# Optimization experiments

Measured on AMD Instinct MI355X. Metric: run time of the kernel, lower is better.

Reference implementation:

```python
import jax, jax.numpy as jnp
import numpy as np

N, F_IN, H, C, E, G, OUT = 50000, 128, 4, 64, 800000, 128, 8

def _glorot(key, shape):
    lim = float(np.sqrt(6.0 / (shape[0] + shape[-1] if len(shape) == 2 else shape[-1] + 1)))
    return jax.random.uniform(key, shape, jnp.float32, -lim, lim)

def setup_inputs() -> dict:
    key = jax.random.key(0)
    ks = jax.random.split(key, 12)
    x = jax.random.normal(ks[0], (N, F_IN), jnp.float32)
    edge_index = jax.random.randint(ks[1], (2, E), 0, N, jnp.int64)
    batch = jnp.sort(jax.random.randint(ks[2], (N,), 0, G, jnp.int64))
    return {
        "x": x, "edge_index": edge_index, "batch": batch,
        "W1": _glorot(ks[3], (F_IN, H * C)),
        "a1s": _glorot(ks[4], (H, C)), "a1d": _glorot(ks[5], (H, C)),
        "b1": jnp.zeros((H * C,), jnp.float32),
        "W2": _glorot(ks[6], (H * C, H * C)),
        "a2s": _glorot(ks[7], (H, C)), "a2d": _glorot(ks[8], (H, C)),
        "b2": jnp.zeros((C,), jnp.float32),
        "fc_w": _glorot(ks[9], (C, OUT)),
        "fc_b": jnp.zeros((OUT,), jnp.float32),
    }

def _gat_conv(x, src, dst, W, a_src, a_dst, bias, concat):
    # x: [N, in]; src/dst: [E'] (self-loops already appended, PyG default)
    n = x.shape[0]
    h = (x @ W).reshape(n, H, C)                       # [N, H, C]
    alpha_src = (h * a_src).sum(-1)                    # [N, H]
    alpha_dst = (h * a_dst).sum(-1)                    # [N, H]
    e = alpha_src[src] + alpha_dst[dst]                # [E', H]
    e = jax.nn.leaky_relu(e, 0.2)
    # neighbor softmax grouped by destination node
    m = jax.ops.segment_max(e, dst, num_segments=n)    # [N, H]
    ex = jnp.exp(e - m[dst])
    denom = jax.ops.segment_sum(ex, dst, num_segments=n)
    alpha = ex / (denom[dst] + 1e-16)                  # [E', H]
    msg = h[src] * alpha[:, :, None]                   # [E', H, C]
    out = jax.ops.segment_sum(msg, dst, num_segments=n)  # [N, H, C]
    out = out.reshape(n, H * C) if concat else out.mean(axis=1)
    return out + bias

def reference(x, edge_index, batch, W1, a1s, a1d, b1, W2, a2s, a2d, b2, fc_w, fc_b):
    n = x.shape[0]
    loop = jnp.arange(n, dtype=edge_index.dtype)
    src = jnp.concatenate([edge_index[0], loop])
    dst = jnp.concatenate([edge_index[1], loop])
    h = _gat_conv(x, src, dst, W1, a1s, a1d, b1, concat=True)
    h = jax.nn.elu(h)                                  # activation, dropout p=0
    h = _gat_conv(h, src, dst, W2, a2s, a2d, b2, concat=False)
    # global mean pool over graphs
    sums = jax.ops.segment_sum(h, batch, num_segments=G)
    cnts = jax.ops.segment_sum(jnp.ones((n,), h.dtype), batch, num_segments=G)
    pooled = sums / jnp.maximum(cnts, 1.0)[:, None]    # [G, C]
    return pooled @ fc_w + fc_b                        # [G, OUT]
```

## Files before the change

kernel.cpp:

```cpp
#include <hip/hip_runtime.h>
#include <hip/hip_bf16.h>
#include <cstddef>
#include <cstdint>

#define NN 50000
#define MPAD 50048
#define F_IN 128
#define NH 4
#define NC 64
#define NE 800000
#define NG 128
#define NOUT 8
#define HC 256
#define EP (NE + NN)
#define NREP 16

typedef unsigned short ushort_t;
typedef _Float16 f16;
typedef __attribute__((ext_vector_type(2))) _Float16 f16x2;
typedef __attribute__((ext_vector_type(8))) _Float16 f16x8;
typedef __attribute__((ext_vector_type(4))) float f32x4;

__device__ __forceinline__ float lrelu02(float x) { return x > 0.0f ? x : 0.2f * x; }
__device__ __forceinline__ float elu1(float x)    { return x > 0.0f ? x : expm1f(x); }

__device__ __forceinline__ ushort_t f2h_bits(float f) {
    f16 h = (f16)f;
    union { f16 h; ushort_t u; } cv; cv.h = h;
    return cv.u;
}
__device__ __forceinline__ uint32_t pack2h(float a, float b) {
    union { f16 h[2]; uint32_t u; } cv;
    cv.h[0] = (f16)a; cv.h[1] = (f16)b;
    return cv.u;
}
__device__ __forceinline__ f16x2 as_h2(uint32_t q) {
    union { uint32_t u; f16x2 h; } cv; cv.u = q;
    return cv.h;
}
__device__ __forceinline__ void h2_unpack(uint32_t q, float& lo, float& hi) {
    union { uint32_t u; f16 h[2]; } cv; cv.u = q;
    lo = (float)cv.h[0];
    hi = (float)cv.h[1];
}

__device__ __forceinline__ float fdot2f(f16x2 a, f16x2 b, float c) {
#if __has_builtin(__builtin_amdgcn_fdot2)
    return __builtin_amdgcn_fdot2(a, b, c, false);
#else
    float d;
    asm("v_dot2_f32_f16 %0, %1, %2, %3" : "=v"(d) : "v"(a), "v"(b), "v"(c));
    return d;
#endif
}
__device__ __forceinline__ uint32_t permb(uint32_t a, uint32_t b, uint32_t s) {
    return __builtin_amdgcn_perm(a, b, s);
}
#define SEL_E 0x01000504u
#define SEL_O 0x03020706u

__device__ __forceinline__ void gld16(const void* g, void* l) {
    __builtin_amdgcn_global_load_lds(
        (const __attribute__((address_space(1))) unsigned int*)g,
        (__attribute__((address_space(3))) unsigned int*)l, 16, 0, 0);
}

#define XN4 (NN * F_IN / 4)
#define NW (F_IN * HC + HC * HC)
__global__ void prep_kernel(const int* __restrict__ edst,
                            const float* __restrict__ x,
                            const float* __restrict__ W1,
                            const float* __restrict__ W2,
                            int* __restrict__ deg,
                            int* __restrict__ rank,
                            f16* __restrict__ xh,
                            f16* __restrict__ w1t, f16* __restrict__ w2t) {
    int idx = blockIdx.x * blockDim.x + threadIdx.x;
    if (idx < EP) {
        int d = (idx < NE) ? edst[idx] : (idx - NE);
        rank[idx] = atomicAdd(&deg[d], 1);
        return;
    }
    idx -= EP;
    if (idx < XN4) {
        float4 v = ((const float4*)x)[idx];
        f16 o[4] = {(f16)v.x, (f16)v.y, (f16)v.z, (f16)v.w};
        *(uint2*)(xh + idx * 4) = *(const uint2*)o;
        return;
    }
    idx -= XN4;
    const int n1 = F_IN * HC;
    if (idx < n1) {
        int k = idx / HC, n = idx % HC;
        w1t[n * F_IN + k] = (f16)W1[idx];
    } else if (idx < NW) {
        int i2 = idx - n1;
        int k = i2 / HC, n = i2 % HC;
        w2t[n * HC + k] = (f16)W2[i2];
    }
}

__global__ __launch_bounds__(256) void scan_p1(const int* __restrict__ deg,
                                               int* __restrict__ partials) {
    __shared__ int lds[256];
    int b = blockIdx.x, t = threadIdx.x;
    int i0 = b * 1024 + t * 4;
    int s = 0;
#pragma unroll
    for (int j = 0; j < 4; j++) { int i = i0 + j; if (i < NN) s += deg[i]; }
    lds[t] = s;
    __syncthreads();
    for (int o = 128; o; o >>= 1) { if (t < o) lds[t] += lds[t + o]; __syncthreads(); }
    if (t == 0) partials[b] = lds[0];
}

__global__ __launch_bounds__(256) void scan_p3(const int* __restrict__ deg,
                                               const int* __restrict__ partials,
                                               int* __restrict__ offs) {
    __shared__ int lds[256];
    __shared__ int base_s;
    int b = blockIdx.x, t = threadIdx.x;
    if (t == 0) {
        int s = 0;
        for (int i = 0; i < b; i++) s += partials[i];
        base_s = s;
        if (b == 0) offs[0] = 0;
    }
    int i0 = b * 1024 + t * 4;
    int v[4]; int s = 0;
#pragma unroll
    for (int j = 0; j < 4; j++) { int i = i0 + j; v[j] = (i < NN) ? deg[i] : 0; s += v[j]; }
    lds[t] = s;
    __syncthreads();
    for (int o = 1; o < 256; o <<= 1) {
        int x = (t >= o) ? lds[t - o] : 0;
        __syncthreads();
        lds[t] += x;
        __syncthreads();
    }
    int run = base_s + (lds[t] - s);
#pragma unroll
    for (int j = 0; j < 4; j++) { run += v[j]; int i = i0 + j; if (i < NN) offs[i + 1] = run; }
}

__global__ void edge_fill(const int* __restrict__ esrc, const int* __restrict__ edst,
                          const int* __restrict__ offs, const int* __restrict__ rank,
                          int* __restrict__ csr) {
    int e = blockIdx.x * blockDim.x + threadIdx.x;
    if (e >= EP) return;
    int s, d;
    if (e < NE) { s = esrc[e]; d = edst[e]; } else { s = d = e - NE; }
    csr[offs[d] + rank[e]] = s;
}

__global__ __launch_bounds__(256, 3) void gemm_gat(
        const f16* __restrict__ A, const f16* __restrict__ BT,
        const float* __restrict__ a_s, const float* __restrict__ a_d,
        ushort_t* __restrict__ hf2, float* __restrict__ asrc,
        float* __restrict__ adst, int M, int K) {
    __shared__ alignas(16) char smem[33792];
    f16* lA = (f16*)smem;
    f16* lB = (f16*)smem + 4096;

    int t = threadIdx.x;
    int wave = t >> 6, lane = t & 63;
    int wm = wave >> 1, wn = wave & 1;
    int quad = lane >> 4, l15 = lane & 15;
    int tileM = blockIdx.x * 128;
    int by = blockIdx.y;

    f32x4 acc[4][4];
#pragma unroll
    for (int f = 0; f < 4; f++)
#pragma unroll
        for (int g = 0; g < 4; g++) acc[f][g] = (f32x4){0.f, 0.f, 0.f, 0.f};

    for (int k0 = 0; k0 < K; k0 += 32) {
        __syncthreads();
#pragma unroll
        for (int i = 0; i < 2; i++) {
            int c = wave * 2 + i;
            int row = c * 16 + (lane >> 2);
            int kk = k0 + (lane & 3) * 8;
            gld16(A + (size_t)(tileM + row) * K + kk, &lA[c * 512]);
            gld16(BT + (size_t)(by * 128 + row) * K + kk, &lB[c * 512]);
        }
        __syncthreads();

        f16x8 ah[4], bh[4];
#pragma unroll
        for (int f = 0; f < 4; f++)
            ah[f] = *(const f16x8*)&lA[(wm * 64 + f * 16 + l15) * 32 + quad * 8];
#pragma unroll
        for (int g = 0; g < 4; g++)
            bh[g] = *(const f16x8*)&lB[(wn * 64 + g * 16 + l15) * 32 + quad * 8];
#pragma unroll
        for (int f = 0; f < 4; f++)
#pragma unroll
            for (int g = 0; g < 4; g++)
                acc[f][g] = __builtin_amdgcn_mfma_f32_16x16x32_f16(ah[f], bh[g], acc[f][g], 0, 0, 0);
    }

    int head = (by << 1) | wn;
    float as_v[4], ad_v[4];
#pragma unroll
    for (int g = 0; g < 4; g++) {
        as_v[g] = a_s[head * 64 + g * 16 + l15];
        ad_v[g] = a_d[head * 64 + g * 16 + l15];
    }
#pragma unroll
    for (int f = 0; f < 4; f++) {
#pragma unroll
        for (int r = 0; r < 4; r++) {
            float ps = acc[f][0][r] * as_v[0] + acc[f][1][r] * as_v[1]
                     + acc[f][2][r] * as_v[2] + acc[f][3][r] * as_v[3];
            float pd = acc[f][0][r] * ad_v[0] + acc[f][1][r] * ad_v[1]
                     + acc[f][2][r] * ad_v[2] + acc[f][3][r] * ad_v[3];
#pragma unroll
            for (int o = 1; o < 16; o <<= 1) {
                ps += __shfl_xor(ps, o);
                pd += __shfl_xor(pd, o);
            }
            int row = tileM + wm * 64 + f * 16 + quad * 4 + r;
            if (l15 == 0 && row < M) {
                asrc[row * 4 + head] = ps;
                adst[row * 4 + head] = pd;
            }
        }
    }

    __syncthreads();
    ushort_t* lC2u = (ushort_t*)smem;
    const uint32_t* lC2d = (const uint32_t*)smem;
#pragma unroll
    for (int f = 0; f < 4; f++)
#pragma unroll
        for (int g = 0; g < 4; g++)
#pragma unroll
            for (int r = 0; r < 4; r++)
                lC2u[(wm * 64 + f * 16 + quad * 4 + r) * 132 + (g * 16 + l15) * 2 + wn] =
                    f2h_bits(acc[f][g][r]);
    __syncthreads();
    uint32_t* hb2 = (uint32_t*)hf2;
#pragma unroll
    for (int it = 0; it < 32; it++) {
        int row = wave * 32 + it;
        uint32_t v = lC2d[row * 66 + lane];
        hb2[(size_t)(tileM + row) * 128 + by * 64 + lane] = v;
    }
}

template <int CONCAT>
__device__ void gat_node_fullwave(const ushort_t* __restrict__ hf2,
                                  const float* __restrict__ asrc,
                                  const float* __restrict__ adst,
                                  const int* __restrict__ offs,
                                  const int* __restrict__ csr,
                                  const int* __restrict__ gb,
                                  const float* __restrict__ bias,
                                  f16* __restrict__ oh,
                                  float* __restrict__ of,
                                  int node, int lane, uint2* lwF) {
    int start = offs[node];
    int deg = offs[node + 1] - start;
    float4 ad = *(const float4*)(adst + node * 4);

    float w0, w1, w2, w3;
    float m0, m1, m2, m3, i0, i1, i2, i3;
    int msrc = 0;

    if (deg <= 64) {
        float t0 = -1e30f, t1 = -1e30f, t2 = -1e30f, t3 = -1e30f;
        if (lane < deg) {
            int sidx = csr[start + lane];
            float4 as = *(const float4*)(asrc + sidx * 4);
            t0 = lrelu02(as.x + ad.x);
            t1 = lrelu02(as.y + ad.y);
            t2 = lrelu02(as.z + ad.z);
            t3 = lrelu02(as.w + ad.w);
            msrc = sidx;
        }
        m0 = t0; m1 = t1; m2 = t2; m3 = t3;
#pragma unroll
        for (int o = 1; o < 64; o <<= 1) {
            m0 = fmaxf(m0, __shfl_xor(m0, o));
            m1 = fmaxf(m1, __shfl_xor(m1, o));
            m2 = fmaxf(m2, __shfl_xor(m2, o));
            m3 = fmaxf(m3, __shfl_xor(m3, o));
        }
        w0 = __expf(t0 - m0);
        w1 = __expf(t1 - m1);
        w2 = __expf(t2 - m2);
        w3 = __expf(t3 - m3);
        float s0 = w0, s1 = w1, s2 = w2, s3 = w3;
#pragma unroll
        for (int o = 1; o < 64; o <<= 1) {
            s0 += __shfl_xor(s0, o);
            s1 += __shfl_xor(s1, o);
            s2 += __shfl_xor(s2, o);
            s3 += __shfl_xor(s3, o);
        }
        i0 = 1.0f / (s0 + 1e-16f);
        i1 = 1.0f / (s1 + 1e-16f);
        i2 = 1.0f / (s2 + 1e-16f);
        i3 = 1.0f / (s3 + 1e-16f);
        w0 *= i0; w1 *= i1; w2 *= i2; w3 *= i3;
    } else {
        m0 = m1 = m2 = m3 = -1e30f;
        float s0 = 0.f, s1 = 0.f, s2 = 0.f, s3 = 0.f;
        float e0 = 0.f, e1 = 0.f, e2 = 0.f, e3 = 0.f;
        for (int j = lane; j < deg; j += 64) {
            int sidx = csr[start + j];
            float4 as = *(const float4*)(asrc + sidx * 4);
            float t0 = lrelu02(as.x + ad.x);
            float t1 = lrelu02(as.y + ad.y);
            float t2 = lrelu02(as.z + ad.z);
            float t3 = lrelu02(as.w + ad.w);
            if (j == lane) { e0 = t0; e1 = t1; e2 = t2; e3 = t3; msrc = sidx; }
            float nm;
            nm = fmaxf(m0, t0); s0 = s0 * __expf(m0 - nm) + __expf(t0 - nm); m0 = nm;
            nm = fmaxf(m1, t1); s1 = s1 * __expf(m1 - nm) + __expf(t1 - nm); m1 = nm;
            nm = fmaxf(m2, t2); s2 = s2 * __expf(m2 - nm) + __expf(t2 - nm); m2 = nm;
            nm = fmaxf(m3, t3); s3 = s3 * __expf(m3 - nm) + __expf(t3 - nm); m3 = nm;
        }
        for (int o = 32; o; o >>= 1) {
            float om, os, nm;
            om = __shfl_xor(m0, o); os = __shfl_xor(s0, o);
            nm = fmaxf(m0, om); s0 = s0 * __expf(m0 - nm) + os * __expf(om - nm); m0 = nm;
            om = __shfl_xor(m1, o); os = __shfl_xor(s1, o);
            nm = fmaxf(m1, om); s1 = s1 * __expf(m1 - nm) + os * __expf(om - nm); m1 = nm;
            om = __shfl_xor(m2, o); os = __shfl_xor(s2, o);
            nm = fmaxf(m2, om); s2 = s2 * __expf(m2 - nm) + os * __expf(om - nm); m2 = nm;
            om = __shfl_xor(m3, o); os = __shfl_xor(s3, o);
            nm = fmaxf(m3, om); s3 = s3 * __expf(m3 - nm) + os * __expf(om - nm); m3 = nm;
        }
        i0 = 1.0f / (s0 + 1e-16f);
        i1 = 1.0f / (s1 + 1e-16f);
        i2 = 1.0f / (s2 + 1e-16f);
        i3 = 1.0f / (s3 + 1e-16f);
        w0 = __expf(e0 - m0) * i0;
        w1 = __expf(e1 - m1) * i1;
        w2 = __expf(e2 - m2) * i2;
        w3 = __expf(e3 - m3) * i3;
    }

    lwF[lane] = (uint2){pack2h(w0, w1), pack2h(w2, w3)};

    int hp = lane >> 5;
    const uint32_t* lwu = (const uint32_t*)lwF;
    float aE0 = 0.f, aO0 = 0.f, aE1 = 0.f, aO1 = 0.f;
    float c0a = 0.f, c0b = 0.f, c1a = 0.f, c1b = 0.f;
    const uint32_t* hb = (const uint32_t*)hf2 + lane * 2;
    int jmax = deg < 64 ? deg : 64;

    int j = 0;
    if (CONCAT) {
        for (; j + 4 <= jmax; j += 4) {
            int s0 = __builtin_amdgcn_readlane(msrc, j);
            int s1 = __builtin_amdgcn_readlane(msrc, j + 1);
            int s2 = __builtin_amdgcn_readlane(msrc, j + 2);
            int s3 = __builtin_amdgcn_readlane(msrc, j + 3);
            uint2 q0 = *(const uint2*)(hb + (size_t)s0 * 128);
            uint2 q1 = *(const uint2*)(hb + (size_t)s1 * 128);
            uint2 q2 = *(const uint2*)(hb + (size_t)s2 * 128);
            uint2 q3 = *(const uint2*)(hb + (size_t)s3 * 128);
            uint32_t wA = lwu[(j + 0) * 2 + hp];
            uint32_t wB = lwu[(j + 1) * 2 + hp];
            uint32_t wC = lwu[(j + 2) * 2 + hp];
            uint32_t wD = lwu[(j + 3) * 2 + hp];
            uint32_t weAB = permb(wA, wB, SEL_E), woAB = permb(wA, wB, SEL_O);
            uint32_t weCD = permb(wC, wD, SEL_E), woCD = permb(wC, wD, SEL_O);
            uint32_t xeAB = permb(q0.x, q1.x, SEL_E), xoAB = permb(q0.x, q1.x, SEL_O);
            uint32_t yeAB = permb(q0.y, q1.y, SEL_E), yoAB = permb(q0.y, q1.y, SEL_O);
            uint32_t xeCD = permb(q2.x, q3.x, SEL_E), xoCD = permb(q2.x, q3.x, SEL_O);
            uint32_t yeCD = permb(q2.y, q3.y, SEL_E), yoCD = permb(q2.y, q3.y, SEL_O);
            aE0 = fdot2f(as_h2(xeAB), as_h2(weAB), aE0);
            aO0 = fdot2f(as_h2(xoAB), as_h2(woAB), aO0);
            aE1 = fdot2f(as_h2(yeAB), as_h2(weAB), aE1);
            aO1 = fdot2f(as_h2(yoAB), as_h2(woAB), aO1);
            aE0 = fdot2f(as_h2(xeCD), as_h2(weCD), aE0);
            aO0 = fdot2f(as_h2(xoCD), as_h2(woCD), aO0);
            aE1 = fdot2f(as_h2(yeCD), as_h2(weCD), aE1);
            aO1 = fdot2f(as_h2(yeCD), as_h2(woCD), aO1);
        }
        for (; j < jmax; j++) {
            int sidx = __builtin_amdgcn_readlane(msrc, j);
            f16x2 wh = as_h2(lwu[j * 2 + hp]);
            uint2 q = *(const uint2*)(hb + (size_t)sidx * 128);
            f16x2 qx = as_h2(q.x), qy = as_h2(q.y);
            aE0 += (float)qx[0] * (float)wh[0];
            aO0 += (float)qx[1] * (float)wh[1];
            aE1 += (float)qy[0] * (float)wh[0];
            aO1 += (float)qy[1] * (float)wh[1];
        }
    } else {
        for (; j + 4 <= jmax; j += 4) {
            int s0 = __builtin_amdgcn_readlane(msrc, j);
            int s1 = __builtin_amdgcn_readlane(msrc, j + 1);
            int s2 = __builtin_amdgcn_readlane(msrc, j + 2);
            int s3 = __builtin_amdgcn_readlane(msrc, j + 3);
            uint2 q0 = *(const uint2*)(hb + (size_t)s0 * 128);
            uint2 q1 = *(const uint2*)(hb + (size_t)s1 * 128);
            uint2 q2 = *(const uint2*)(hb + (size_t)s2 * 128);
            uint2 q3 = *(const uint2*)(hb + (size_t)s3 * 128);
            f16x2 w0v = as_h2(lwu[(j + 0) * 2 + hp]);
            f16x2 w1v = as_h2(lwu[(j + 1) * 2 + hp]);
            f16x2 w2v = as_h2(lwu[(j + 2) * 2 + hp]);
            f16x2 w3v = as_h2(lwu[(j + 3) * 2 + hp]);
            c0a = fdot2f(as_h2(q0.x), w0v, c0a);
            c1a = fdot2f(as_h2(q0.y), w0v, c1a);
            c0b = fdot2f(as_h2(q1.x), w1v, c0b);
            c1b = fdot2f(as_h2(q1.y), w1v, c1b);
            c0a = fdot2f(as_h2(q2.x), w2v, c0a);
            c1a = fdot2f(as_h2(q2.y), w2v, c1a);
            c0b = fdot2f(as_h2(q3.x), w3v, c0b);
            c1b = fdot2f(as_h2(q3.y), w3v, c1b);
        }
        for (; j < jmax; j++) {
            int sidx = __builtin_amdgcn_readlane(msrc, j);
            f16x2 wh = as_h2(lwu[j * 2 + hp]);
            uint2 q = *(const uint2*)(hb + (size_t)sidx * 128);
            c0a = fdot2f(as_h2(q.x), wh, c0a);
            c1a = fdot2f(as_h2(q.y), wh, c1a);
        }
    }
    for (int jj = 64; jj < deg; jj++) {
        int sidx = csr[start + jj];
        float4 as = *(const float4*)(asrc + sidx * 4);
        float u0 = __expf(lrelu02(as.x + ad.x) - m0) * i0;
        float u1 = __expf(lrelu02(as.y + ad.y) - m1) * i1;
        float u2 = __expf(lrelu02(as.z + ad.z) - m2) * i2;
        float u3 = __expf(lrelu02(as.w + ad.w) - m3) * i3;
        float ue = hp ? u2 : u0;
        float uo = hp ? u3 : u1;
        uint2 q = *(const uint2*)(hb + (size_t)sidx * 128);
        float xl, xh2, yl, yh;
        h2_unpack(q.x, xl, xh2);
        h2_unpack(q.y, yl, yh);
        if (CONCAT) {
            aE0 += ue * xl;
            aO0 += uo * xh2;
            aE1 += ue * yl;
            aO1 += uo * yh;
        } else {
            c0a += ue * xl + uo * xh2;
            c1a += ue * yl + uo * yh;
        }
    }

    int c0 = (lane & 31) * 2;
    int he = hp * 2, ho = hp * 2 + 1;
    if (CONCAT) {
        size_t base = (size_t)node * HC;
        float vE0 = elu1(aE0 + bias[he * 64 + c0]);
        float vE1 = elu1(aE1 + bias[he * 64 + c0 + 1]);
        float vO0 = elu1(aO0 + bias[ho * 64 + c0]);
        float vO1 = elu1(aO1 + bias[ho * 64 + c0 + 1]);
        f16 pe[2] = {(f16)vE0, (f16)vE1};
        f16 po[2] = {(f16)vO0, (f16)vO1};
        *(uint32_t*)(oh + base + he * 64 + c0) = *(const uint32_t*)pe;
        *(uint32_t*)(oh + base + ho * 64 + c0) = *(const uint32_t*)po;
    } else {
        float s0 = c0a + c0b;
        float s1 = c1a + c1b;
        s0 += __shfl_xor(s0, 32);
        s1 += __shfl_xor(s1, 32);
        if (hp == 0) {
            int g = gb[node];
            atomicAdd(of + g * 64 + c0, 0.25f * s0);
            atomicAdd(of + g * 64 + c0 + 1, 0.25f * s1);
        }
    }
}

template <int CONCAT>
__global__ __launch_bounds__(256, 4) void gat_agg(const ushort_t* __restrict__ hf2,
                                                  const float* __restrict__ asrc,
                                                  const float* __restrict__ adst,
                                                  const int* __restrict__ offs,
                                                  const int* __restrict__ csr,
                                                  const int* __restrict__ gb,
                                                  const float* __restrict__ bias,
                                                  f16* __restrict__ oh,
                                                  float* __restrict__ of) {
    __shared__ uint4 lw4[4][64];
    __shared__ float part[2][64];
    __shared__ int oks[4];
    int wave = threadIdx.x >> 6, lane = threadIdx.x & 63;
    int grp = lane >> 5, l31 = lane & 31;
    int hp = (lane >> 4) & 1;
    int nbase = blockIdx.x * 8 + wave * 2;
    int node = nbase + grp;
    int start = offs[node];
    int deg = offs[node + 1] - start;

    float* ofr = of + (size_t)(blockIdx.x & (NREP - 1)) * NG * 64;

    bool ok = __all(deg <= 32);
    bool useLds = false;
    int g_first = 0, g_last = 0;
    if (!CONCAT) {
        if (threadIdx.x < 128) ((float*)part)[threadIdx.x] = 0.f;
        if (lane == 0) oks[wave] = ok ? 1 : 0;
        __syncthreads();
        useLds = oks[0] && oks[1] && oks[2] && oks[3];
        g_first = gb[blockIdx.x * 8];
        g_last  = gb[blockIdx.x * 8 + 7];
    }

    if (!ok) {
        uint2* lwF = (uint2*)&lw4[wave][0];
        gat_node_fullwave<CONCAT>(hf2, asrc, adst, offs, csr, gb, bias, oh, ofr,
                                  nbase, lane, lwF);
        gat_node_fullwave<CONCAT>(hf2, asrc, adst, offs, csr, gb, bias, oh, ofr,
                                  nbase + 1, lane, lwF);
        return;
    }

    const uint4* hq = (const uint4*)hf2;
    int msrc = 0;
    bool act = l31 < deg;
    if (act) msrc = csr[start + l31];

    int b0 = grp * 32;
    int i0 = __shfl(msrc, b0 + 0);
    int i1 = __shfl(msrc, b0 + 1);
    int i2 = __shfl(msrc, b0 + 2);
    int i3 = __shfl(msrc, b0 + 3);
    int i4 = __shfl(msrc, b0 + 4);
    int i5 = __shfl(msrc, b0 + 5);
    int i6 = __shfl(msrc, b0 + 6);
    int i7 = __shfl(msrc, b0 + 7);
    uint4 q0 = hq[(uint32_t)i0 * 32u + l31];
    uint4 q1 = hq[(uint32_t)i1 * 32u + l31];
    uint4 q2 = hq[(uint32_t)i2 * 32u + l31];
    uint4 q3 = hq[(uint32_t)i3 * 32u + l31];
    uint4 r0 = hq[(uint32_t)i4 * 32u + l31];
    uint4 r1 = hq[(uint32_t)i5 * 32u + l31];
    uint4 r2 = hq[(uint32_t)i6 * 32u + l31];
    uint4 r3 = hq[(uint32_t)i7 * 32u + l31];

    float4 ad = *(const float4*)(adst + (size_t)node * 4);
    float t0 = -1e30f, t1 = -1e30f, t2 = -1e30f, t3 = -1e30f;
    if (act) {
        float4 as = *(const float4*)(asrc + (size_t)msrc * 4);
        t0 = lrelu02(as.x + ad.x);
        t1 = lrelu02(as.y + ad.y);
        t2 = lrelu02(as.z + ad.z);
        t3 = lrelu02(as.w + ad.w);
    }
    float m0 = t0, m1 = t1, m2 = t2, m3 = t3;
#pragma unroll
    for (int o = 1; o < 32; o <<= 1) {
        m0 = fmaxf(m0, __shfl_xor(m0, o));
        m1 = fmaxf(m1, __shfl_xor(m1, o));
        m2 = fmaxf(m2, __shfl_xor(m2, o));
        m3 = fmaxf(m3, __shfl_xor(m3, o));
    }
    float w0 = __expf(t0 - m0);
    float w1 = __expf(t1 - m1);
    float w2 = __expf(t2 - m2);
    float w3 = __expf(t3 - m3);
    float s0 = w0, s1 = w1, s2 = w2, s3 = w3;
#pragma unroll
    for (int o = 1; o < 32; o <<= 1) {
        s0 += __shfl_xor(s0, o);
        s1 += __shfl_xor(s1, o);
        s2 += __shfl_xor(s2, o);
        s3 += __shfl_xor(s3, o);
    }
    w0 *= 1.0f / (s0 + 1e-16f);
    w1 *= 1.0f / (s1 + 1e-16f);
    w2 *= 1.0f / (s2 + 1e-16f);
    w3 *= 1.0f / (s3 + 1e-16f);

    lw4[wave][lane] = (uint4){(uint32_t)msrc, pack2h(w0, w1),
                              (uint32_t)msrc, pack2h(w2, w3)};

    const uint2* lwp = (const uint2*)&lw4[wave][grp * 32];
    int c0 = (l31 & 15) * 4;
    int deg4 = (deg + 3) & ~3;

    uint32_t wy0 = lwp[0 * 2 + hp].y;
    uint32_t wy1 = lwp[1 * 2 + hp].y;
    uint32_t wy2 = lwp[2 * 2 + hp].y;
    uint32_t wy3 = lwp[3 * 2 + hp].y;
    uint32_t wz0 = lwp[4 * 2 + hp].y;
    uint32_t wz1 = lwp[5 * 2 + hp].y;
    uint32_t wz2 = lwp[6 * 2 + hp].y;
    uint32_t wz3 = lwp[7 * 2 + hp].y;

    if (CONCAT) {
        float aE0 = 0.f, aE1 = 0.f, aE2 = 0.f, aE3 = 0.f;
        float aO0 = 0.f, aO1 = 0.f, aO2 = 0.f, aO3 = 0.f;
#define CPAIR(A0, A1, W0, W1)                                                  \
        {                                                                      \
            uint32_t we = permb(W0, W1, SEL_E);                                \
            uint32_t wo = permb(W0, W1, SEL_O);                                \
            aE0 = fdot2f(as_h2(permb(A0.x, A1.x, SEL_E)), as_h2(we), aE0);     \
            aO0 = fdot2f(as_h2(permb(A0.x, A1.x, SEL_O)), as_h2(wo), aO0);     \
            aE1 = fdot2f(as_h2(permb(A0.y, A1.y, SEL_E)), as_h2(we), aE1);     \
            aO1 = fdot2f(as_h2(permb(A0.y, A1.y, SEL_O)), as_h2(wo), aO1);     \
            aE2 = fdot2f(as_h2(permb(A0.z, A1.z, SEL_E)), as_h2(we), aE2);     \
            aO2 = fdot2f(as_h2(permb(A0.z, A1.z, SEL_O)), as_h2(wo), aO2);     \
            aE3 = fdot2f(as_h2(permb(A0.w, A1.w, SEL_E)), as_h2(we), aE3);     \
            aO3 = fdot2f(as_h2(permb(A0.w, A1.w, SEL_O)), as_h2(wo), aO3);     \
        }
        int j = 0;
        for (;;) {
            CPAIR(q0, q1, wy0, wy1)
            CPAIR(q2, q3, wy2, wy3)
            {
                int p = j + 8;
                if (p < deg4) {
                    uint2 n0 = lwp[(p + 0) * 2 + hp];
                    uint2 n1 = lwp[(p + 1) * 2 + hp];
                    uint2 n2 = lwp[(p + 2) * 2 + hp];
                    uint2 n3 = lwp[(p + 3) * 2 + hp];
                    wy0 = n0.y; wy1 = n1.y; wy2 = n2.y; wy3 = n3.y;
                    q0 = hq[n0.x * 32u + l31];
                    q1 = hq[n1.x * 32u + l31];
                    q2 = hq[n2.x * 32u + l31];
                    q3 = hq[n3.x * 32u + l31];
                }
            }
            j += 4;
            if (j >= deg4) break;
            CPAIR(r0, r1, wz0, wz1)
            CPAIR(r2, r3, wz2, wz3)
            {
                int p = j + 8;
                if (p < deg4) {
                    uint2 n0 = lwp[(p + 0) * 2 + hp];
                    uint2 n1 = lwp[(p + 1) * 2 + hp];
                    uint2 n2 = lwp[(p + 2) * 2 + hp];
                    uint2 n3 = lwp[(p + 3) * 2 + hp];
                    wz0 = n0.y; wz1 = n1.y; wz2 = n2.y; wz3 = n3.y;
                    r0 = hq[n0.x * 32u + l31];
                    r1 = hq[n1.x * 32u + l31];
                    r2 = hq[n2.x * 32u + l31];
                    r3 = hq[n3.x * 32u + l31];
                }
            }
            j += 4;
            if (j >= deg4) break;
        }
#undef CPAIR
        int he = hp * 2, ho = hp * 2 + 1;
        size_t base = (size_t)node * HC;
        float4 bE = *(const float4*)(bias + he * 64 + c0);
        float4 bO = *(const float4*)(bias + ho * 64 + c0);
        f16 pe[4] = {(f16)elu1(aE0 + bE.x), (f16)elu1(aE1 + bE.y),
                     (f16)elu1(aE2 + bE.z), (f16)elu1(aE3 + bE.w)};
        f16 po[4] = {(f16)elu1(aO0 + bO.x), (f16)elu1(aO1 + bO.y),
                     (f16)elu1(aO2 + bO.z), (f16)elu1(aO3 + bO.w)};
        *(uint2*)(oh + base + he * 64 + c0) = *(const uint2*)pe;
        *(uint2*)(oh + base + ho * 64 + c0) = *(const uint2*)po;
    } else {
        float a0 = 0.f, a1 = 0.f, a2 = 0.f, a3 = 0.f;
        float b0f = 0.f, b1f = 0.f, b2f = 0.f, b3f = 0.f;
        int j = 0;
        for (;;) {
            {
                f16x2 wvA = as_h2(wy0), wvB = as_h2(wy1);
                f16x2 wvC = as_h2(wy2), wvD = as_h2(wy3);
                a0 = fdot2f(as_h2(q0.x), wvA, a0);
                a1 = fdot2f(as_h2(q0.y), wvA, a1);
                a2 = fdot2f(as_h2(q0.z), wvA, a2);
                a3 = fdot2f(as_h2(q0.w), wvA, a3);
                b0f = fdot2f(as_h2(q1.x), wvB, b0f);
                b1f = fdot2f(as_h2(q1.y), wvB, b1f);
                b2f = fdot2f(as_h2(q1.z), wvB, b2f);
                b3f = fdot2f(as_h2(q1.w), wvB, b3f);
                a0 = fdot2f(as_h2(q2.x), wvC, a0);
                a1 = fdot2f(as_h2(q2.y), wvC, a1);
                a2 = fdot2f(as_h2(q2.z), wvC, a2);
                a3 = fdot2f(as_h2(q2.w), wvC, a3);
                b0f = fdot2f(as_h2(q3.x), wvD, b0f);
                b1f = fdot2f(as_h2(q3.y), wvD, b1f);
                b2f = fdot2f(as_h2(q3.z), wvD, b2f);
                b3f = fdot2f(as_h2(q3.w), wvD, b3f);
            }
            {
                int p = j + 8;
                if (p < deg4) {
                    uint2 n0 = lwp[(p + 0) * 2 + hp];
                    uint2 n1 = lwp[(p + 1) * 2 + hp];
                    uint2 n2 = lwp[(p + 2) * 2 + hp];
                    uint2 n3 = lwp[(p + 3) * 2 + hp];
                    wy0 = n0.y; wy1 = n1.y; wy2 = n2.y; wy3 = n3.y;
                    q0 = hq[n0.x * 32u + l31];
                    q1 = hq[n1.x * 32u + l31];
                    q2 = hq[n2.x * 32u + l31];
                    q3 = hq[n3.x * 32u + l31];
                }
            }
            j += 4;
            if (j >= deg4) break;
            {
                f16x2 wvA = as_h2(wz0), wvB = as_h2(wz1);
                f16x2 wvC = as_h2(wz2), wvD = as_h2(wz3);
                a0 = fdot2f(as_h2(r0.x), wvA, a0);
                a1 = fdot2f(as_h2(r0.y), wvA, a1);
                a2 = fdot2f(as_h2(r0.z), wvA, a2);
                a3 = fdot2f(as_h2(r0.w), wvA, a3);
                b0f = fdot2f(as_h2(r1.x), wvB, b0f);
                b1f = fdot2f(as_h2(r1.y), wvB, b1f);
                b2f = fdot2f(as_h2(r1.z), wvB, b2f);
                b3f = fdot2f(as_h2(r1.w), wvB, b3f);
                a0 = fdot2f(as_h2(r2.x), wvC, a0);
                a1 = fdot2f(as_h2(r2.y), wvC, a1);
                a2 = fdot2f(as_h2(r2.z), wvC, a2);
                a3 = fdot2f(as_h2(r2.w), wvC, a3);
                b0f = fdot2f(as_h2(r3.x), wvD, b0f);
                b1f = fdot2f(as_h2(r3.y), wvD, b1f);
                b2f = fdot2f(as_h2(r3.z), wvD, b2f);
                b3f = fdot2f(as_h2(r3.w), wvD, b3f);
            }
            {
                int p = j + 8;
                if (p < deg4) {
                    uint2 n0 = lwp[(p + 0) * 2 + hp];
                    uint2 n1 = lwp[(p + 1) * 2 + hp];
                    uint2 n2 = lwp[(p + 2) * 2 + hp];
                    uint2 n3 = lwp[(p + 3) * 2 + hp];
                    wz0 = n0.y; wz1 = n1.y; wz2 = n2.y; wz3 = n3.y;
                    r0 = hq[n0.x * 32u + l31];
                    r1 = hq[n1.x * 32u + l31];
                    r2 = hq[n2.x * 32u + l31];
                    r3 = hq[n3.x * 32u + l31];
                }
            }
            j += 4;
            if (j >= deg4) break;
        }
        float u0 = a0 + b0f, u1 = a1 + b1f, u2 = a2 + b2f, u3 = a3 + b3f;
        u0 += __shfl_xor(u0, 16);
        u1 += __shfl_xor(u1, 16);
        u2 += __shfl_xor(u2, 16);
        u3 += __shfl_xor(u3, 16);
        float o0 = 0.25f * u0, o1 = 0.25f * u1, o2 = 0.25f * u2, o3 = 0.25f * u3;
        int g = gb[node];
        if (hp == 0) {
            bool inLds = useLds && (g == g_first || g == g_last);
            if (inLds) {
                int slot = (g != g_first) ? 1 : 0;
                atomicAdd(&part[slot][c0 + 0], o0);
                atomicAdd(&part[slot][c0 + 1], o1);
                atomicAdd(&part[slot][c0 + 2], o2);
                atomicAdd(&part[slot][c0 + 3], o3);
            } else {
                float* pb = ofr + g * 64 + c0;
                atomicAdd(pb + 0, o0);
                atomicAdd(pb + 1, o1);
                atomicAdd(pb + 2, o2);
                atomicAdd(pb + 3, o3);
            }
        }
        if (useLds) {
            __syncthreads();
            int t = threadIdx.x;
            if (t < 64) {
                atomicAdd(ofr + g_first * 64 + t, part[0][t]);
            } else if (t < 128 && g_last != g_first) {
                atomicAdd(ofr + g_last * 64 + (t - 64), part[1][t - 64]);
            }
        }
    }
}

__global__ void fc_kernel(const float* __restrict__ pool,
                          const int* __restrict__ batch,
                          const float* __restrict__ b2,
                          const float* __restrict__ fc_w, const float* __restrict__ fc_b,
                          float* __restrict__ out) {
    int idx = blockIdx.x * blockDim.x + threadIdx.x;
    if (idx >= NG * NOUT) return;
    int g = idx >> 3, o = idx & 7;
    int lo = 0, hi = NN;
    while (lo < hi) { int mid = (lo + hi) >> 1; if (batch[mid] < g) lo = mid + 1; else hi = mid; }
    int lo2 = lo, hi2 = NN;
    while (lo2 < hi2) { int mid = (lo2 + hi2) >> 1; if (batch[mid] < g + 1) lo2 = mid + 1; else hi2 = mid; }
    float inv = 1.0f / fmaxf((float)(lo2 - lo), 1.0f);
    float s = 0.f;
#pragma unroll
    for (int c = 0; c < 64; c++) {
        float v = 0.f;
#pragma unroll
        for (int r = 0; r < NREP; r++) v += pool[((size_t)r * NG + g) * 64 + c];
        s += (v * inv + b2[c]) * fc_w[c * 8 + o];
    }
    out[idx] = s + fc_b[o];
}

extern "C" void kernel_launch(void* const* d_in, const int* in_sizes, int n_in,
                              void* d_out, int out_size, void* d_ws, size_t ws_size,
                              hipStream_t stream) {
    const float* x    = (const float*)d_in[0];
    const int*   ei   = (const int*)d_in[1];
    const int*   batch= (const int*)d_in[2];
    const float* W1   = (const float*)d_in[3];
    const float* a1s  = (const float*)d_in[4];
    const float* a1d  = (const float*)d_in[5];
    const float* b1   = (const float*)d_in[6];
    const float* W2   = (const float*)d_in[7];
    const float* a2s  = (const float*)d_in[8];
    const float* a2d  = (const float*)d_in[9];
    const float* b2   = (const float*)d_in[10];
    const float* fc_w = (const float*)d_in[11];
    const float* fc_b = (const float*)d_in[12];
    float* out = (float*)d_out;

    char* p = (char*)d_ws;
    auto alloc = [&](size_t bytes) -> char* {
        char* r = p; p += (bytes + 255) & ~(size_t)255; return r;
    };
    int*   deg     = (int*)alloc((size_t)NN * 4);
    float* pool    = (float*)alloc((size_t)NREP * NG * 64 * 4);
    size_t zero_bytes = (size_t)(p - (char*)d_ws);
    int*   offs    = (int*)alloc((size_t)(NN + 1) * 4);
    int*   partials= (int*)alloc(64 * 4);
    int*   csr     = (int*)alloc((size_t)EP * 4);
    int*   rank    = (int*)alloc((size_t)EP * 4);
    float* asrc    = (float*)alloc((size_t)NN * 4 * 4);
    float* adst    = (float*)alloc((size_t)NN * 4 * 4);
    ushort_t* hf2  = (ushort_t*)alloc((size_t)MPAD * HC * 2);
    f16*   xh      = (f16*)alloc((size_t)MPAD * F_IN * 2);
    f16*   act     = (f16*)alloc((size_t)MPAD * HC * 2);
    f16*   w1t     = (f16*)alloc((size_t)HC * F_IN * 2);
    f16*   w2t     = (f16*)alloc((size_t)HC * HC * 2);

    hipMemsetAsync(d_ws, 0, zero_bytes, stream);

    int prep_n = EP + XN4 + NW;
    prep_kernel<<<(prep_n + 255) / 256, 256, 0, stream>>>(
        ei + NE, x, W1, W2, deg, rank, xh, w1t, w2t);
    scan_p1<<<49, 256, 0, stream>>>(deg, partials);
    scan_p3<<<49, 256, 0, stream>>>(deg, partials, offs);
    edge_fill<<<(EP + 255) / 256, 256, 0, stream>>>(ei, ei + NE, offs, rank, csr);

    dim3 gg((NN + 127) / 128, HC / 128);
    int nb8 = (NN + 7) / 8;

    gemm_gat<<<gg, 256, 0, stream>>>(xh, w1t, a1s, a1d, hf2, asrc, adst, NN, F_IN);
    gat_agg<1><<<nb8, 256, 0, stream>>>(hf2, asrc, adst, offs, csr, batch, b1, act, nullptr);
    gemm_gat<<<gg, 256, 0, stream>>>(act, w2t, a2s, a2d, hf2, asrc, adst, NN, HC);
    gat_agg<0><<<nb8, 256, 0, stream>>>(hf2, asrc, adst, offs, csr, batch, b2, nullptr, pool);
    fc_kernel<<<(NG * NOUT + 255) / 256, 256, 0, stream>>>(pool, batch, b2, fc_w, fc_b, out);
}
```

Measured before the change: 346.1 us.

## Fuse CSR edge fill into first GEMM launch and widen GEMM K-tile with swizzle

Removes the separate edge_fill launch by appending extra blocks to the first gemm_gat grid that scatter edges into the CSR array, so the fill runs alongside the layer-1 GEMM. The GEMM K step doubles from 32 to 64 with an XOR-swizzled LDS layout to cut barriers per K and avoid LDS bank conflicts, and the grid becomes 1D. It also fixes a wrong operand (ye instead of yo) in the unrolled aggregation dot product, which changes the numerical result.

```diff
diff --git a/kernel.cpp b/kernel.cpp
--- a/kernel.cpp
+++ b/kernel.cpp
@@ -143,31 +143,36 @@
     for (int j = 0; j < 4; j++) { run += v[j]; int i = i0 + j; if (i < NN) offs[i + 1] = run; }
 }
 
-__global__ void edge_fill(const int* __restrict__ esrc, const int* __restrict__ edst,
-                          const int* __restrict__ offs, const int* __restrict__ rank,
-                          int* __restrict__ csr) {
-    int e = blockIdx.x * blockDim.x + threadIdx.x;
-    if (e >= EP) return;
-    int s, d;
-    if (e < NE) { s = esrc[e]; d = edst[e]; } else { s = d = e - NE; }
-    csr[offs[d] + rank[e]] = s;
-}
-
 __global__ __launch_bounds__(256, 3) void gemm_gat(
         const f16* __restrict__ A, const f16* __restrict__ BT,
         const float* __restrict__ a_s, const float* __restrict__ a_d,
         ushort_t* __restrict__ hf2, float* __restrict__ asrc,
-        float* __restrict__ adst, int M, int K) {
+        float* __restrict__ adst, int M, int K, int gemmBlocks,
+        const int* __restrict__ esrc, const int* __restrict__ edst,
+        const int* __restrict__ offs, const int* __restrict__ rank,
+        int* __restrict__ csr) {
     __shared__ alignas(16) char smem[33792];
+
+    int bid = blockIdx.x;
+    if (bid >= gemmBlocks) {
+        int e = (bid - gemmBlocks) * 256 + threadIdx.x;
+        if (e < EP) {
+            int s, d;
+            if (e < NE) { s = esrc[e]; d = edst[e]; } else { s = d = e - NE; }
+            csr[offs[d] + rank[e]] = s;
+        }
+        return;
+    }
+
     f16* lA = (f16*)smem;
-    f16* lB = (f16*)smem + 4096;
+    f16* lB = (f16*)smem + 8192;
 
     int t = threadIdx.x;
     int wave = t >> 6, lane = t & 63;
     int wm = wave >> 1, wn = wave & 1;
     int quad = lane >> 4, l15 = lane & 15;
-    int tileM = blockIdx.x * 128;
-    int by = blockIdx.y;
+    int tileM = (bid >> 1) * 128;
+    int by = bid & 1;
 
     f32x4 acc[4][4];
 #pragma unroll
@@ -175,30 +180,39 @@
 #pragma unroll
         for (int g = 0; g < 4; g++) acc[f][g] = (f32x4){0.f, 0.f, 0.f, 0.f};
 
-    for (int k0 = 0; k0 < K; k0 += 32) {
+    int swl = ((lane & 7) ^ (lane >> 3)) * 8;
+    int rsw = l15 & 7;
+
+    for (int k0 = 0; k0 < K; k0 += 64) {
         __syncthreads();
 #pragma unroll
-        for (int i = 0; i < 2; i++) {
-            int c = wave * 2 + i;
-            int row = c * 16 + (lane >> 2);
-            int kk = k0 + (lane & 3) * 8;
+        for (int i = 0; i < 4; i++) {
+            int c = wave * 4 + i;
+            int row = c * 8 + (lane >> 3);
+            int kk = k0 + swl;
             gld16(A + (size_t)(tileM + row) * K + kk, &lA[c * 512]);
             gld16(BT + (size_t)(by * 128 + row) * K + kk, &lB[c * 512]);
         }
         __syncthreads();
 
-        f16x8 ah[4], bh[4];
-#pragma unroll
-        for (int f = 0; f < 4; f++)
-            ah[f] = *(const f16x8*)&lA[(wm * 64 + f * 16 + l15) * 32 + quad * 8];
-#pragma unroll
-        for (int g = 0; g < 4; g++)
-            bh[g] = *(const f16x8*)&lB[(wn * 64 + g * 16 + l15) * 32 + quad * 8];
-#pragma unroll
-        for (int f = 0; f < 4; f++)
+#pragma unroll
+        for (int h = 0; h < 2; h++) {
+            f16x8 ah[4], bh[4];
+#pragma unroll
+            for (int f = 0; f < 4; f++)
+                ah[f] = *(const f16x8*)&lA[(wm * 64 + f * 16 + l15) * 64 +
+                                           (((h * 4 + quad) ^ rsw) * 8)];
 #pragma unroll
             for (int g = 0; g < 4; g++)
-                acc[f][g] = __builtin_amdgcn_mfma_f32_16x16x32_f16(ah[f], bh[g], acc[f][g], 0, 0, 0);
+                bh[g] = *(const f16x8*)&lB[(wn * 64 + g * 16 + l15) * 64 +
+                                           (((h * 4 + quad) ^ rsw) * 8)];
+#pragma unroll
+            for (int f = 0; f < 4; f++)
+#pragma unroll
+                for (int g = 0; g < 4; g++)
+                    acc[f][g] = __builtin_amdgcn_mfma_f32_16x16x32_f16(
+                        ah[f], bh[g], acc[f][g], 0, 0, 0);
+        }
     }
 
     int head = (by << 1) | wn;
@@ -381,7 +395,7 @@
             aE0 = fdot2f(as_h2(xeCD), as_h2(weCD), aE0);
             aO0 = fdot2f(as_h2(xoCD), as_h2(woCD), aO0);
             aE1 = fdot2f(as_h2(yeCD), as_h2(weCD), aE1);
-            aO1 = fdot2f(as_h2(yeCD), as_h2(woCD), aO1);
+            aO1 = fdot2f(as_h2(yoCD), as_h2(woCD), aO1);
         }
         for (; j < jmax; j++) {
             int sidx = __builtin_amdgcn_readlane(msrc, j);
@@ -837,14 +851,18 @@
         ei + NE, x, W1, W2, deg, rank, xh, w1t, w2t);
     scan_p1<<<49, 256, 0, stream>>>(deg, partials);
     scan_p3<<<49, 256, 0, stream>>>(deg, partials, offs);
-    edge_fill<<<(EP + 255) / 256, 256, 0, stream>>>(ei, ei + NE, offs, rank, csr);
-
-    dim3 gg((NN + 127) / 128, HC / 128);
+
+    int gemmB = ((NN + 127) / 128) * 2;
+    int fillB = (EP + 255) / 256;
     int nb8 = (NN + 7) / 8;
 
-    gemm_gat<<<gg, 256, 0, stream>>>(xh, w1t, a1s, a1d, hf2, asrc, adst, NN, F_IN);
+    gemm_gat<<<gemmB + fillB, 256, 0, stream>>>(
+        xh, w1t, a1s, a1d, hf2, asrc, adst, NN, F_IN, gemmB,
+        ei, ei + NE, offs, rank, csr);
     gat_agg<1><<<nb8, 256, 0, stream>>>(hf2, asrc, adst, offs, csr, batch, b1, act, nullptr);
-    gemm_gat<<<gg, 256, 0, stream>>>(act, w2t, a2s, a2d, hf2, asrc, adst, NN, HC);
+    gemm_gat<<<gemmB, 256, 0, stream>>>(
+        act, w2t, a2s, a2d, hf2, asrc, adst, NN, HC, gemmB,
+        ei, ei + NE, offs, rank, csr);
     gat_agg<0><<<nb8, 256, 0, stream>>>(hf2, asrc, adst, offs, csr, batch, b2, nullptr, pool);
     fc_kernel<<<(NG * NOUT + 255) / 256, 256, 0, stream>>>(pool, batch, b2, fc_w, fc_b, out);
 }
```

Result: faster. 334.4 us (median of 2 runs) (-3.4%).
